# Performance work log

Measured on AMD Instinct MI355X. Metric: run time of the kernel, lower is better.

The kernel has to match this reference:

```python
import jax, jax.numpy as jnp
import numpy as np

T, D, H = 2048, 2048, 16
C = D // H  # head dim = 128

def setup_inputs() -> dict:
    key = jax.random.key(0)
    k1, k2, k3 = jax.random.split(key, 3)
    x = jax.random.normal(k1, (T, D), dtype=jnp.float32)
    W_attn = jax.random.normal(k2, (3 * D, D), dtype=jnp.float32) * 0.02
    W_proj = jax.random.normal(k3, (D, D), dtype=jnp.float32) * 0.02
    return {"x": x, "W_attn": W_attn, "W_proj": W_proj}

def reference(x, W_attn, W_proj):
    # c_attn: per-token Linear -> [T, 3D]
    qkv = x @ W_attn.T
    q, k, v = jnp.split(qkv, 3, axis=-1)  # each [T, D]
    # [T, D] -> [H, T, C]
    q = q.reshape(T, H, C).transpose(1, 0, 2)
    k = k.reshape(T, H, C).transpose(1, 0, 2)
    v = v.reshape(T, H, C).transpose(1, 0, 2)
    # raw scores [H, T, T]
    scores = jnp.einsum('htc,hsc->hts', q, k)
    causal_mask = jnp.tril(jnp.ones((1, T, T))) == 0
    scores = jnp.where(causal_mask, float('-inf'), scores)
    orig_dtype = scores.dtype
    # NOTE: original scales AFTER masking, inside softmax, in fp32
    attn = jax.nn.softmax(scores.astype(jnp.float32) / jnp.sqrt(jnp.float32(C)), axis=-1)
    attn = attn.astype(orig_dtype)
    out = attn @ v  # [H, T, C]
    out = out.transpose(1, 0, 2).reshape(T, D)
    return out @ W_proj.T
```

## Files before the change

kernel.cpp:

```cpp
#include <hip/hip_runtime.h>
#include <hip/hip_bf16.h>
#include <stdint.h>

typedef __attribute__((ext_vector_type(8))) __bf16 bf16x8;
typedef __attribute__((ext_vector_type(4))) float f32x4;
typedef __attribute__((ext_vector_type(4))) unsigned int u32x4;
typedef __attribute__((ext_vector_type(4))) unsigned short u16x4;

__device__ __forceinline__ unsigned short f2bf(float f) {
  union { float f; unsigned int u; } v; v.f = f;
  unsigned int r = v.u + 0x7fffu + ((v.u >> 16) & 1u);
  return (unsigned short)(r >> 16);
}

__global__ __launch_bounds__(256) void cast_f32_bf16(const float* __restrict__ in,
                                                     unsigned short* __restrict__ out,
                                                     int n) {
  int i = (blockIdx.x * 256 + threadIdx.x) * 4;
  if (i >= n) return;
  f32x4 v = *(const f32x4*)&in[i];
  u16x4 o;
  o[0] = f2bf(v[0]); o[1] = f2bf(v[1]); o[2] = f2bf(v[2]); o[3] = f2bf(v[3]);
  *(u16x4*)&out[i] = o;
}

template<int OUT_BF16>
__global__ __launch_bounds__(256, 2) void gemm_bt(const unsigned short* __restrict__ A,
                                                  const unsigned short* __restrict__ B,
                                                  void* __restrict__ Cv,
                                                  int M, int N, int K) {
  __shared__ unsigned short As[128][40];
  __shared__ unsigned short Bs[128][40];

  const int tid  = threadIdx.x;
  const int lane = tid & 63;
  const int wave = tid >> 6;
  const int wr = (wave >> 1) * 64;
  const int wc = (wave & 1) * 64;
  const int row0 = blockIdx.y * 128;
  const int col0 = blockIdx.x * 128;

  const int l16 = lane & 15;
  const int lk  = (lane >> 4) * 8;

  const int srow = tid >> 2;
  const int sc   = (tid & 3) * 8;

  f32x4 acc[4][4] = {};

  for (int k0 = 0; k0 < K; k0 += 32) {
    __syncthreads();
    u32x4 a0 = *(const u32x4*)&A[(size_t)(row0 + srow) * K + k0 + sc];
    u32x4 a1 = *(const u32x4*)&A[(size_t)(row0 + 64 + srow) * K + k0 + sc];
    u32x4 b0 = *(const u32x4*)&B[(size_t)(col0 + srow) * K + k0 + sc];
    u32x4 b1 = *(const u32x4*)&B[(size_t)(col0 + 64 + srow) * K + k0 + sc];
    *(u32x4*)&As[srow][sc]      = a0;
    *(u32x4*)&As[64 + srow][sc] = a1;
    *(u32x4*)&Bs[srow][sc]      = b0;
    *(u32x4*)&Bs[64 + srow][sc] = b1;
    __syncthreads();

    bf16x8 af[4], bfr[4];
#pragma unroll
    for (int i = 0; i < 4; ++i) af[i]  = *(const bf16x8*)&As[wr + i * 16 + l16][lk];
#pragma unroll
    for (int i = 0; i < 4; ++i) bfr[i] = *(const bf16x8*)&Bs[wc + i * 16 + l16][lk];
#pragma unroll
    for (int i = 0; i < 4; ++i)
#pragma unroll
      for (int j = 0; j < 4; ++j)
        acc[i][j] = __builtin_amdgcn_mfma_f32_16x16x32_bf16(af[i], bfr[j], acc[i][j], 0, 0, 0);
  }

  const int orow = (lane >> 4) * 4;
#pragma unroll
  for (int i = 0; i < 4; ++i)
#pragma unroll
    for (int j = 0; j < 4; ++j)
#pragma unroll
      for (int r = 0; r < 4; ++r) {
        size_t gr = row0 + wr + i * 16 + orow + r;
        size_t gc = col0 + wc + j * 16 + l16;
        float v = acc[i][j][r];
        if (OUT_BF16) ((unsigned short*)Cv)[gr * N + gc] = f2bf(v);
        else          ((float*)Cv)[gr * N + gc] = v;
      }
}

__global__ __launch_bounds__(256, 2) void attn_kernel(const unsigned short* __restrict__ qkv,
                                                      unsigned short* __restrict__ ctx) {
  __shared__ unsigned short Ks[64][136];
  __shared__ unsigned short VTs[128][72];
  __shared__ unsigned short Ps[4][16][72];

  const int tid  = threadIdx.x;
  const int lane = tid & 63;
  const int w    = tid >> 6;
  const int h    = blockIdx.y;
  const int qb   = blockIdx.x;
  const int l16  = lane & 15;
  const int lk8  = (lane >> 4) * 8;
  const int qrow = qb * 64 + w * 16;

  bf16x8 qf[4];
#pragma unroll
  for (int kk = 0; kk < 4; ++kk)
    qf[kk] = *(const bf16x8*)&qkv[(size_t)(qrow + l16) * 6144 + h * 128 + kk * 32 + lk8];

  f32x4 o[8] = {};
  float m[4], lsum[4];
#pragma unroll
  for (int r = 0; r < 4; ++r) { m[r] = -1e30f; lsum[r] = 0.f; }

  const float sscale = 0.08838834764831845f * 1.4426950408889634f;
  const int qg0 = qrow + (lane >> 4) * 4;

  const int nkb = qb + 1;
  for (int kb = 0; kb < nkb; ++kb) {
    __syncthreads();
#pragma unroll
    for (int it = 0; it < 4; ++it) {
      int idx = it * 256 + tid;
      int row = idx >> 4, c0 = (idx & 15) * 8;
      *(u32x4*)&Ks[row][c0] =
          *(const u32x4*)&qkv[(size_t)(kb * 64 + row) * 6144 + 2048 + h * 128 + c0];
    }
#pragma unroll
    for (int it = 0; it < 4; ++it) {
      int idx = it * 256 + tid;
      int t = idx & 63, c0 = (idx >> 6) * 8;
      u32x4 vv = *(const u32x4*)&qkv[(size_t)(kb * 64 + t) * 6144 + 4096 + h * 128 + c0];
      const unsigned short* pv = (const unsigned short*)&vv;
#pragma unroll
      for (int j = 0; j < 8; ++j) VTs[c0 + j][t] = pv[j];
    }
    __syncthreads();

    f32x4 s[4] = {};
#pragma unroll
    for (int kk = 0; kk < 4; ++kk)
#pragma unroll
      for (int n = 0; n < 4; ++n) {
        bf16x8 kf = *(const bf16x8*)&Ks[n * 16 + l16][kk * 32 + lk8];
        s[n] = __builtin_amdgcn_mfma_f32_16x16x32_bf16(qf[kk], kf, s[n], 0, 0, 0);
      }

    const bool diag = (kb == qb);
    float rmax[4];
#pragma unroll
    for (int r = 0; r < 4; ++r) rmax[r] = -1e30f;
#pragma unroll
    for (int n = 0; n < 4; ++n) {
      int kg = kb * 64 + n * 16 + l16;
#pragma unroll
      for (int r = 0; r < 4; ++r) {
        float v = s[n][r] * sscale;
        if (diag && kg > qg0 + r) v = -1e30f;
        s[n][r] = v;
        rmax[r] = fmaxf(rmax[r], v);
      }
    }
#pragma unroll
    for (int d = 1; d < 16; d <<= 1)
#pragma unroll
      for (int r = 0; r < 4; ++r) rmax[r] = fmaxf(rmax[r], __shfl_xor(rmax[r], d));

    float alpha[4];
#pragma unroll
    for (int r = 0; r < 4; ++r) {
      float mn = fmaxf(m[r], rmax[r]);
      alpha[r] = exp2f(m[r] - mn);
      m[r] = mn;
    }
    float rsum[4] = {0.f, 0.f, 0.f, 0.f};
#pragma unroll
    for (int n = 0; n < 4; ++n)
#pragma unroll
      for (int r = 0; r < 4; ++r) {
        float p = exp2f(s[n][r] - m[r]);
        s[n][r] = p;
        rsum[r] += p;
      }
#pragma unroll
    for (int d = 1; d < 16; d <<= 1)
#pragma unroll
      for (int r = 0; r < 4; ++r) rsum[r] += __shfl_xor(rsum[r], d);
#pragma unroll
    for (int r = 0; r < 4; ++r) lsum[r] = lsum[r] * alpha[r] + rsum[r];

#pragma unroll
    for (int n = 0; n < 8; ++n)
#pragma unroll
      for (int r = 0; r < 4; ++r) o[n][r] *= alpha[r];

#pragma unroll
    for (int n = 0; n < 4; ++n)
#pragma unroll
      for (int r = 0; r < 4; ++r)
        Ps[w][(lane >> 4) * 4 + r][n * 16 + l16] = f2bf(s[n][r]);
    __syncthreads();

#pragma unroll
    for (int kk = 0; kk < 2; ++kk) {
      bf16x8 pf = *(const bf16x8*)&Ps[w][l16][kk * 32 + lk8];
#pragma unroll
      for (int n = 0; n < 8; ++n) {
        bf16x8 vf = *(const bf16x8*)&VTs[n * 16 + l16][kk * 32 + lk8];
        o[n] = __builtin_amdgcn_mfma_f32_16x16x32_bf16(pf, vf, o[n], 0, 0, 0);
      }
    }
  }

#pragma unroll
  for (int r = 0; r < 4; ++r) {
    float inv = 1.0f / lsum[r];
    size_t gr = qrow + (lane >> 4) * 4 + r;
#pragma unroll
    for (int n = 0; n < 8; ++n)
      ctx[gr * 2048 + h * 128 + n * 16 + l16] = f2bf(o[n][r] * inv);
  }
}

extern "C" void kernel_launch(void* const* d_in, const int* in_sizes, int n_in,
                              void* d_out, int out_size, void* d_ws, size_t ws_size,
                              hipStream_t stream) {
  const float* x  = (const float*)d_in[0];
  const float* Wa = (const float*)d_in[1];
  const float* Wp = (const float*)d_in[2];
  float* out = (float*)d_out;

  char* ws = (char*)d_ws;
  unsigned short* xb   = (unsigned short*)(ws);
  unsigned short* wab  = (unsigned short*)(ws + 8388608);
  unsigned short* wpb  = (unsigned short*)(ws + 33554432);
  unsigned short* qkvb = (unsigned short*)(ws + 41943040);
  unsigned short* ctx  = (unsigned short*)(ws + 67108864);

  cast_f32_bf16<<<4096, 256, 0, stream>>>(x, xb, 2048 * 2048);
  cast_f32_bf16<<<12288, 256, 0, stream>>>(Wa, wab, 6144 * 2048);
  cast_f32_bf16<<<4096, 256, 0, stream>>>(Wp, wpb, 2048 * 2048);

  gemm_bt<1><<<dim3(48, 16), 256, 0, stream>>>(xb, wab, qkvb, 2048, 6144, 2048);

  attn_kernel<<<dim3(32, 16), 256, 0, stream>>>(qkvb, ctx);

  gemm_bt<0><<<dim3(16, 16), 256, 0, stream>>>(ctx, wpb, out, 2048, 2048, 2048);
}
```

Baseline: 339.0 us.

## Use direct global-to-LDS loads in GEMM, rebalance and restage attention loads

The GEMM tiles now load through global_load_lds into unpadded shared memory, which skips the register round-trip. The launch_bounds occupancy hint is dropped. The attention kernel remaps blocks so heads 8-15 run query blocks in reverse order, to balance causal work across CUs. It also issues K/V global loads before the barrier into registers and transposes V with 4-element vector LDS writes instead of scalar writes. In exchange, the unpadded GEMM LDS layout may bring back bank conflicts on fragment reads, and the extra registers may lower occupancy.

```diff
diff --git a/kernel.cpp b/kernel.cpp
--- a/kernel.cpp
+++ b/kernel.cpp
@@ -11,6 +11,12 @@
   union { float f; unsigned int u; } v; v.f = f;
   unsigned int r = v.u + 0x7fffu + ((v.u >> 16) & 1u);
   return (unsigned short)(r >> 16);
+}
+
+__device__ __forceinline__ void gload_lds16(const void* g, void* l) {
+  __builtin_amdgcn_global_load_lds(
+      (const __attribute__((address_space(1))) unsigned int*)g,
+      (__attribute__((address_space(3))) unsigned int*)l, 16, 0, 0);
 }
 
 __global__ __launch_bounds__(256) void cast_f32_bf16(const float* __restrict__ in,
@@ -25,12 +31,12 @@
 }
 
 template<int OUT_BF16>
-__global__ __launch_bounds__(256, 2) void gemm_bt(const unsigned short* __restrict__ A,
-                                                  const unsigned short* __restrict__ B,
-                                                  void* __restrict__ Cv,
-                                                  int M, int N, int K) {
-  __shared__ unsigned short As[128][40];
-  __shared__ unsigned short Bs[128][40];
+__global__ __launch_bounds__(256) void gemm_bt(const unsigned short* __restrict__ A,
+                                               const unsigned short* __restrict__ B,
+                                               void* __restrict__ Cv,
+                                               int M, int N, int K) {
+  __shared__ unsigned short As[128 * 32];
+  __shared__ unsigned short Bs[128 * 32];
 
   const int tid  = threadIdx.x;
   const int lane = tid & 63;
@@ -39,32 +45,30 @@
   const int wc = (wave & 1) * 64;
   const int row0 = blockIdx.y * 128;
   const int col0 = blockIdx.x * 128;
-
   const int l16 = lane & 15;
   const int lk  = (lane >> 4) * 8;
 
-  const int srow = tid >> 2;
-  const int sc   = (tid & 3) * 8;
+  const int srow = lane >> 2;
+  const int sc   = (lane & 3) * 8;
 
   f32x4 acc[4][4] = {};
 
   for (int k0 = 0; k0 < K; k0 += 32) {
     __syncthreads();
-    u32x4 a0 = *(const u32x4*)&A[(size_t)(row0 + srow) * K + k0 + sc];
-    u32x4 a1 = *(const u32x4*)&A[(size_t)(row0 + 64 + srow) * K + k0 + sc];
-    u32x4 b0 = *(const u32x4*)&B[(size_t)(col0 + srow) * K + k0 + sc];
-    u32x4 b1 = *(const u32x4*)&B[(size_t)(col0 + 64 + srow) * K + k0 + sc];
-    *(u32x4*)&As[srow][sc]      = a0;
-    *(u32x4*)&As[64 + srow][sc] = a1;
-    *(u32x4*)&Bs[srow][sc]      = b0;
-    *(u32x4*)&Bs[64 + srow][sc] = b1;
+#pragma unroll
+    for (int i = 0; i < 2; ++i) {
+      int t = wave * 2 + i;
+      int r = t * 16 + srow;
+      gload_lds16(&A[(size_t)(row0 + r) * K + k0 + sc], &As[t * 512]);
+      gload_lds16(&B[(size_t)(col0 + r) * K + k0 + sc], &Bs[t * 512]);
+    }
     __syncthreads();
 
     bf16x8 af[4], bfr[4];
 #pragma unroll
-    for (int i = 0; i < 4; ++i) af[i]  = *(const bf16x8*)&As[wr + i * 16 + l16][lk];
-#pragma unroll
-    for (int i = 0; i < 4; ++i) bfr[i] = *(const bf16x8*)&Bs[wc + i * 16 + l16][lk];
+    for (int i = 0; i < 4; ++i) af[i]  = *(const bf16x8*)&As[(wr + i * 16 + l16) * 32 + lk];
+#pragma unroll
+    for (int i = 0; i < 4; ++i) bfr[i] = *(const bf16x8*)&Bs[(wc + i * 16 + l16) * 32 + lk];
 #pragma unroll
     for (int i = 0; i < 4; ++i)
 #pragma unroll
@@ -96,10 +100,14 @@
   const int tid  = threadIdx.x;
   const int lane = tid & 63;
   const int w    = tid >> 6;
-  const int h    = blockIdx.y;
-  const int qb   = blockIdx.x;
   const int l16  = lane & 15;
   const int lk8  = (lane >> 4) * 8;
+
+  const int flat = blockIdx.x + blockIdx.y * 32;
+  int h, qb;
+  if (flat < 256) { h = flat >> 5; qb = flat & 31; }
+  else            { int f2 = flat - 256; h = 8 + (f2 >> 5); qb = 31 - (f2 & 31); }
+
   const int qrow = qb * 64 + w * 16;
 
   bf16x8 qf[4];
@@ -115,24 +123,40 @@
   const float sscale = 0.08838834764831845f * 1.4426950408889634f;
   const int qg0 = qrow + (lane >> 4) * 4;
 
+  const int t0v = (tid & 15) * 4;
+  const int c0v = (tid >> 4) * 8;
+
   const int nkb = qb + 1;
   for (int kb = 0; kb < nkb; ++kb) {
-    __syncthreads();
+    u32x4 kreg[4], vreg[4];
 #pragma unroll
     for (int it = 0; it < 4; ++it) {
       int idx = it * 256 + tid;
       int row = idx >> 4, c0 = (idx & 15) * 8;
-      *(u32x4*)&Ks[row][c0] =
-          *(const u32x4*)&qkv[(size_t)(kb * 64 + row) * 6144 + 2048 + h * 128 + c0];
-    }
+      kreg[it] = *(const u32x4*)&qkv[(size_t)(kb * 64 + row) * 6144 + 2048 + h * 128 + c0];
+    }
+#pragma unroll
+    for (int r = 0; r < 4; ++r)
+      vreg[r] = *(const u32x4*)&qkv[(size_t)(kb * 64 + t0v + r) * 6144 + 4096 + h * 128 + c0v];
+
+    __syncthreads();
+
 #pragma unroll
     for (int it = 0; it < 4; ++it) {
       int idx = it * 256 + tid;
-      int t = idx & 63, c0 = (idx >> 6) * 8;
-      u32x4 vv = *(const u32x4*)&qkv[(size_t)(kb * 64 + t) * 6144 + 4096 + h * 128 + c0];
-      const unsigned short* pv = (const unsigned short*)&vv;
-#pragma unroll
-      for (int j = 0; j < 8; ++j) VTs[c0 + j][t] = pv[j];
+      int row = idx >> 4, c0 = (idx & 15) * 8;
+      *(u32x4*)&Ks[row][c0] = kreg[it];
+    }
+    {
+      const unsigned short* p0 = (const unsigned short*)&vreg[0];
+      const unsigned short* p1 = (const unsigned short*)&vreg[1];
+      const unsigned short* p2 = (const unsigned short*)&vreg[2];
+      const unsigned short* p3 = (const unsigned short*)&vreg[3];
+#pragma unroll
+      for (int j = 0; j < 8; ++j) {
+        u16x4 wv; wv[0] = p0[j]; wv[1] = p1[j]; wv[2] = p2[j]; wv[3] = p3[j];
+        *(u16x4*)&VTs[c0v + j][t0v] = wv;
+      }
     }
     __syncthreads();
 
```

Result: faster. 313.0 us (-7.6%).
